# Optimization experiments

Hardware: AMD Instinct MI355X
Metric: run time of the kernel (lower is better)

The kernel has to match this reference:

```python
import jax, jax.numpy as jnp
import numpy as np

F_DIM, P_DIM, H_DIM, N_EXP = 768, 512, 1024, 4
B, T = 8192, 8192


def _gelu(x):
    return jax.nn.gelu(x, approximate=False)


def _normalize(x, eps=1e-12):
    n = jnp.linalg.norm(x, axis=-1, keepdims=True)
    return x / jnp.maximum(n, eps)


def setup_inputs() -> dict:
    key = jax.random.key(0)
    ks = jax.random.split(key, 24)
    s = 0.02
    inp = {
        'image_features': jax.random.normal(ks[0], (B, F_DIM), jnp.float32),
        'text_features': jax.random.normal(ks[1], (B, F_DIM), jnp.float32),
        'target_features': jax.random.normal(ks[2], (T, F_DIM), jnp.float32),
        # projection layers (torch Linear convention: W [out,in])
        'Wt': jax.random.normal(ks[3], (P_DIM, F_DIM), jnp.float32) * s,
        'bt': jnp.zeros((P_DIM,), jnp.float32),
        'Wi': jax.random.normal(ks[4], (P_DIM, F_DIM), jnp.float32) * s,
        'bi': jnp.zeros((P_DIM,), jnp.float32),
        # dynamic scalar MLP: (2P -> H -> 1)
        'ds_W1': jax.random.normal(ks[5], (H_DIM, 2 * P_DIM), jnp.float32) * s,
        'ds_b1': jnp.zeros((H_DIM,), jnp.float32),
        'ds_W2': jax.random.normal(ks[6], (1, H_DIM), jnp.float32) * s,
        'ds_b2': jnp.zeros((1,), jnp.float32),
        # experts stacked: [E, H, 2P]
        'exp_W': jax.random.normal(ks[7], (N_EXP, H_DIM, 2 * P_DIM), jnp.float32) * s,
        'exp_b': jnp.zeros((N_EXP, H_DIM), jnp.float32),
        # router: (2P -> H/4 -> E)
        'rt_W1': jax.random.normal(ks[8], (H_DIM // 4, 2 * P_DIM), jnp.float32) * s,
        'rt_b1': jnp.zeros((H_DIM // 4,), jnp.float32),
        'rt_W2': jax.random.normal(ks[9], (N_EXP, H_DIM // 4), jnp.float32) * s,
        'rt_b2': jnp.zeros((N_EXP,), jnp.float32),
        # output layer: (H -> F)
        'out_W': jax.random.normal(ks[10], (F_DIM, H_DIM), jnp.float32) * s,
        'out_b': jnp.zeros((F_DIM,), jnp.float32),
        'logit_scale': jnp.asarray(np.log(50.0), jnp.float32),
    }
    return inp


def reference(image_features, text_features, target_features, Wt, bt, Wi, bi,
              ds_W1, ds_b1, ds_W2, ds_b2, exp_W, exp_b,
              rt_W1, rt_b1, rt_W2, rt_b2, out_W, out_b, logit_scale):
    # eval mode: all dropouts are identity, no modality drop
    tp = _gelu(text_features @ Wt.T + bt)            # [B,P]
    ip = _gelu(image_features @ Wi.T + bi)           # [B,P]
    comb = jnp.concatenate([tp, ip], axis=-1)        # [B,2P]

    router_logits = _gelu(comb @ rt_W1.T + rt_b1) @ rt_W2.T + rt_b2  # [B,E]
    router_probs = jax.nn.softmax(router_logits, axis=-1)

    expert_out = _gelu(jnp.einsum('bd,ehd->beh', comb, exp_W) + exp_b)  # [B,E,H]
    fused_hidden = jnp.einsum('be,beh->bh', router_probs, expert_out)   # [B,H]
    residual = fused_hidden @ out_W.T + out_b                            # [B,F]

    ds = jax.nn.sigmoid(_gelu(comb @ ds_W1.T + ds_b1) @ ds_W2.T + ds_b2)  # [B,1]
    output = ds * text_features + (1.0 - ds) * image_features + residual
    pred = _normalize(output)
    tgt = _normalize(target_features)
    logits = jnp.exp(logit_scale) * (pred @ tgt.T)   # [B,T]
    return (logits, ds, router_probs)
```

## Files before the change

### kernel.cpp

```cpp
#include <hip/hip_runtime.h>
#include <stdint.h>
#include <math.h>

#define BDIM 8192
#define TDIM 8192
#define FDIM 768
#define PDIM 512
#define HDIM 1024
#define NEXP 4
#define NCAT 5376

using short4v = __attribute__((ext_vector_type(4))) short;
using short8 = __attribute__((ext_vector_type(8))) short;
using f32x4  = __attribute__((ext_vector_type(4))) float;

__device__ __forceinline__ short f2bf(float f) {
  uint32_t u = __builtin_bit_cast(uint32_t, f);
  u += 0x7fffu + ((u >> 16) & 1u);
  return (short)(u >> 16);
}
__device__ __forceinline__ float bf2f(short s) {
  uint32_t u = ((uint32_t)(uint16_t)s) << 16;
  return __builtin_bit_cast(float, u);
}
__device__ __forceinline__ float gelu_exact(float x) {
  return 0.5f * x * (1.0f + erff(x * 0.70710678118654752f));
}

#define GLDS(gp, lp) __builtin_amdgcn_global_load_lds( \
    (const __attribute__((address_space(1))) void*)(gp), \
    (__attribute__((address_space(3))) void*)(lp), 16, 0, 0)

template <int MODE>
__device__ __forceinline__ void gemm_body(
    const short* __restrict__ A, int lda,
    const short* __restrict__ B, int ldb,
    void* __restrict__ C, int ldc, int K,
    const float* __restrict__ bias, float scale,
    int m0, int n0)
{
  __shared__ short sA[4096];
  __shared__ short sB[4096];
  const int t    = threadIdx.x;
  const int lane = t & 63;
  const int wave = t >> 6;
  const int wm = (wave >> 1) * 64;
  const int wn = (wave & 1) * 64;
  const int l15  = lane & 15;
  const int quad = lane >> 4;

  f32x4 acc[4][4];
#pragma unroll
  for (int i = 0; i < 4; ++i)
#pragma unroll
    for (int j = 0; j < 4; ++j)
      acc[i][j] = (f32x4){0.f, 0.f, 0.f, 0.f};

  const int rr = t >> 2;
  const int cc = (t & 3) * 8;
  const short* gA0 = A + (size_t)(m0 + rr) * lda + cc;
  const short* gA1 = A + (size_t)(m0 + 64 + rr) * lda + cc;
  const short* gB0 = B + (size_t)(n0 + rr) * ldb + cc;
  const short* gB1 = B + (size_t)(n0 + 64 + rr) * ldb + cc;
  short* lA0 = sA + t * 8;
  short* lA1 = sA + 2048 + t * 8;
  short* lB0 = sB + t * 8;
  short* lB1 = sB + 2048 + t * 8;

  for (int k0 = 0; k0 < K; k0 += 32) {
    GLDS(gA0 + k0, lA0);
    GLDS(gA1 + k0, lA1);
    GLDS(gB0 + k0, lB0);
    GLDS(gB1 + k0, lB1);
    __syncthreads();
    short8 af[4], bfr[4];
#pragma unroll
    for (int i = 0; i < 4; ++i)
      af[i] = *(const short8*)(sA + (wm + i * 16 + l15) * 32 + quad * 8);
#pragma unroll
    for (int j = 0; j < 4; ++j)
      bfr[j] = *(const short8*)(sB + (wn + j * 16 + l15) * 32 + quad * 8);
#pragma unroll
    for (int i = 0; i < 4; ++i)
#pragma unroll
      for (int j = 0; j < 4; ++j)
        acc[i][j] = __builtin_amdgcn_mfma_f32_16x16x32_bf16(af[i], bfr[j], acc[i][j], 0, 0, 0);
    __syncthreads();
  }

#pragma unroll
  for (int i = 0; i < 4; ++i) {
#pragma unroll
    for (int j = 0; j < 4; ++j) {
      const int col = n0 + wn + j * 16 + l15;
      float bv = (MODE == 2) ? 0.f : bias[col];
#pragma unroll
      for (int r = 0; r < 4; ++r) {
        const int row = m0 + wm + i * 16 + quad * 4 + r;
        float v = acc[i][j][r];
        if (MODE == 0) {
          v = gelu_exact(v + bv);
          ((short*)C)[(size_t)row * ldc + col] = f2bf(v);
        } else if (MODE == 1) {
          ((float*)C)[(size_t)row * ldc + col] = v + bv;
        } else {
          ((float*)C)[(size_t)row * ldc + col] = v * scale;
        }
      }
    }
  }
}

template <int MODE>
__global__ __launch_bounds__(256, 2)
void gemm_bt(const short* __restrict__ A, int lda,
             const short* __restrict__ B, int ldb,
             void* __restrict__ C, int ldc, int K,
             const float* __restrict__ bias,
             const float* __restrict__ scale_ptr)
{
  float scale = 1.f;
  if (MODE == 2) scale = expf(scale_ptr[0]);
  gemm_body<MODE>(A, lda, B, ldb, C, ldc, K, bias, scale,
                  blockIdx.y * 128, blockIdx.x * 128);
}

__global__ __launch_bounds__(256, 2)
void gemm_proj(const short* __restrict__ textb, const short* __restrict__ imgb,
               const short* __restrict__ Wtb, const short* __restrict__ Wib,
               const float* __restrict__ bt, const float* __restrict__ bi,
               short* __restrict__ comb)
{
  const int z = blockIdx.z;
  const short* A = z ? imgb : textb;
  const short* B = z ? Wib : Wtb;
  const float* bias = z ? bi : bt;
  short* C = comb + (z ? 512 : 0);
  gemm_body<0>(A, FDIM, B, FDIM, C, 1024, FDIM, bias, 1.f,
               blockIdx.y * 128, blockIdx.x * 128);
}

#define SEG0 1572864u
#define SEG1 3145728u
#define SEG2 3244032u
#define SEG3 3342336u
#define SEG4 4390912u
#define SEG5 4653056u
#define SEG6 4718592u
#define SEG7 4915200u
#define SEG8 4916544u

__global__ __launch_bounds__(256)
void prep_all(const float* __restrict__ text, const float* __restrict__ image,
              const float* __restrict__ Wt, const float* __restrict__ Wi,
              const float* __restrict__ exp_W, const float* __restrict__ ds_W1,
              const float* __restrict__ rt_W1, const float* __restrict__ out_W,
              const float* __restrict__ exp_b, const float* __restrict__ ds_b1,
              const float* __restrict__ rt_b1,
              short* __restrict__ textb, short* __restrict__ imgb,
              short* __restrict__ Wtb, short* __restrict__ Wib,
              short* __restrict__ Bcat, short* __restrict__ outWb,
              float* __restrict__ biascat)
{
  const uint32_t i = blockIdx.x * 256 + threadIdx.x;
  if (i >= SEG8) return;
  if (i >= SEG7) {
    const uint32_t j = (i - SEG7) * 4;
#pragma unroll
    for (int k = 0; k < 4; ++k) {
      uint32_t idx = j + k;
      float v;
      if (idx < 4096)      v = exp_b[idx];
      else if (idx < 5120) v = ds_b1[idx - 4096];
      else                 v = rt_b1[idx - 5120];
      biascat[idx] = v;
    }
    return;
  }
  const float* s;
  short* d;
  uint32_t j;
  if (i < SEG1) {
    if (i < SEG0) { j = i;        s = text;  d = textb; }
    else          { j = i - SEG0; s = image; d = imgb;  }
  } else if (i < SEG3) {
    if (i < SEG2) { j = i - SEG1; s = Wt; d = Wtb; }
    else          { j = i - SEG2; s = Wi; d = Wib; }
  } else if (i < SEG5) {
    if (i < SEG4) { j = i - SEG3; s = exp_W; d = Bcat; }
    else          { j = i - SEG4; s = ds_W1; d = Bcat + (size_t)4096 * 1024; }
  } else {
    if (i < SEG6) { j = i - SEG5; s = rt_W1; d = Bcat + (size_t)5120 * 1024; }
    else          { j = i - SEG6; s = out_W; d = outWb; }
  }
  float4 v = ((const float4*)s)[j];
  short4v o = { f2bf(v.x), f2bf(v.y), f2bf(v.z), f2bf(v.w) };
  ((short4v*)d)[j] = o;
}

__global__ __launch_bounds__(256)
void moe_mix(const short* __restrict__ Hall,
             const float* __restrict__ rt_W2, const float* __restrict__ rt_b2,
             const float* __restrict__ ds_W2, const float* __restrict__ ds_b2,
             float* __restrict__ out_probs, float* __restrict__ out_ds,
             short* __restrict__ fused)
{
  const int b = blockIdx.x;
  const int t = threadIdx.x;
  const int lane = t & 63;
  const int wave = t >> 6;
  const short* h = Hall + (size_t)b * NCAT;

  float rv = bf2f(h[5120 + t]);
  float p0 = rv * rt_W2[t];
  float p1 = rv * rt_W2[256 + t];
  float p2 = rv * rt_W2[512 + t];
  float p3 = rv * rt_W2[768 + t];
  float dd = 0.f;
#pragma unroll
  for (int k = 0; k < 4; ++k)
    dd += bf2f(h[4096 + k * 256 + t]) * ds_W2[k * 256 + t];

#pragma unroll
  for (int off = 32; off; off >>= 1) {
    p0 += __shfl_xor(p0, off);
    p1 += __shfl_xor(p1, off);
    p2 += __shfl_xor(p2, off);
    p3 += __shfl_xor(p3, off);
    dd += __shfl_xor(dd, off);
  }
  __shared__ float red[5][4];
  __shared__ float bc[5];
  if (lane == 0) {
    red[0][wave] = p0; red[1][wave] = p1; red[2][wave] = p2;
    red[3][wave] = p3; red[4][wave] = dd;
  }
  __syncthreads();
  if (t == 0) {
    float l0 = red[0][0] + red[0][1] + red[0][2] + red[0][3] + rt_b2[0];
    float l1 = red[1][0] + red[1][1] + red[1][2] + red[1][3] + rt_b2[1];
    float l2 = red[2][0] + red[2][1] + red[2][2] + red[2][3] + rt_b2[2];
    float l3 = red[3][0] + red[3][1] + red[3][2] + red[3][3] + rt_b2[3];
    float d  = red[4][0] + red[4][1] + red[4][2] + red[4][3] + ds_b2[0];
    float mx = fmaxf(fmaxf(l0, l1), fmaxf(l2, l3));
    float e0 = expf(l0 - mx), e1 = expf(l1 - mx);
    float e2 = expf(l2 - mx), e3 = expf(l3 - mx);
    float inv = 1.f / (e0 + e1 + e2 + e3);
    bc[0] = e0 * inv; bc[1] = e1 * inv; bc[2] = e2 * inv; bc[3] = e3 * inv;
    bc[4] = 1.f / (1.f + expf(-d));
    out_probs[b * 4 + 0] = bc[0];
    out_probs[b * 4 + 1] = bc[1];
    out_probs[b * 4 + 2] = bc[2];
    out_probs[b * 4 + 3] = bc[3];
    out_ds[b] = bc[4];
  }
  __syncthreads();
  const float q0 = bc[0], q1 = bc[1], q2 = bc[2], q3 = bc[3];
  short* fr = fused + (size_t)b * 1024;
#pragma unroll
  for (int c = t; c < 1024; c += 256) {
    float v = q0 * bf2f(h[c])        + q1 * bf2f(h[1024 + c])
            + q2 * bf2f(h[2048 + c]) + q3 * bf2f(h[3072 + c]);
    fr[c] = f2bf(v);
  }
}

__global__ __launch_bounds__(256)
void normalize_both(const float* __restrict__ text, const float* __restrict__ image,
                    const float* __restrict__ ds, const float* __restrict__ resid,
                    const float* __restrict__ target,
                    short* __restrict__ pred, short* __restrict__ tgtb)
{
  const int bb = blockIdx.x;
  const int t = threadIdx.x;
  float o0, o1, o2;
  short* d;
  if (bb < BDIM) {
    const float dv = ds[bb];
    const float* tx = text + (size_t)bb * FDIM;
    const float* im = image + (size_t)bb * FDIM;
    const float* s  = resid + (size_t)bb * FDIM;
    o0 = dv * tx[t]       + (1.f - dv) * im[t]       + s[t];
    o1 = dv * tx[t + 256] + (1.f - dv) * im[t + 256] + s[t + 256];
    o2 = dv * tx[t + 512] + (1.f - dv) * im[t + 512] + s[t + 512];
    d = pred + (size_t)bb * FDIM;
  } else {
    const int b = bb - BDIM;
    const float* s = target + (size_t)b * FDIM;
    o0 = s[t]; o1 = s[t + 256]; o2 = s[t + 512];
    d = tgtb + (size_t)b * FDIM;
  }
  float ss = o0 * o0 + o1 * o1 + o2 * o2;
  __shared__ float red[4];
#pragma unroll
  for (int off = 32; off; off >>= 1) ss += __shfl_xor(ss, off);
  if ((t & 63) == 0) red[t >> 6] = ss;
  __syncthreads();
  const float tot = red[0] + red[1] + red[2] + red[3];
  const float rn = 1.f / fmaxf(sqrtf(tot), 1e-12f);
  d[t]       = f2bf(o0 * rn);
  d[t + 256] = f2bf(o1 * rn);
  d[t + 512] = f2bf(o2 * rn);
}

extern "C" void kernel_launch(void* const* d_in, const int* in_sizes, int n_in,
                              void* d_out, int out_size, void* d_ws, size_t ws_size,
                              hipStream_t stream) {
  const float* image  = (const float*)d_in[0];
  const float* text   = (const float*)d_in[1];
  const float* target = (const float*)d_in[2];
  const float* Wt     = (const float*)d_in[3];
  const float* bt     = (const float*)d_in[4];
  const float* Wi     = (const float*)d_in[5];
  const float* bi     = (const float*)d_in[6];
  const float* ds_W1  = (const float*)d_in[7];
  const float* ds_b1  = (const float*)d_in[8];
  const float* ds_W2  = (const float*)d_in[9];
  const float* ds_b2  = (const float*)d_in[10];
  const float* exp_W  = (const float*)d_in[11];
  const float* exp_b  = (const float*)d_in[12];
  const float* rt_W1  = (const float*)d_in[13];
  const float* rt_b1  = (const float*)d_in[14];
  const float* rt_W2  = (const float*)d_in[15];
  const float* rt_b2  = (const float*)d_in[16];
  const float* out_W  = (const float*)d_in[17];
  const float* out_b  = (const float*)d_in[18];
  const float* logit_scale = (const float*)d_in[19];

  char* ws = (char*)d_ws;
  short* comb  = (short*)ws;  ws += (size_t)BDIM * 1024 * 2;
  short* Hall  = (short*)ws;  ws += (size_t)BDIM * NCAT * 2;
  short* fused = (short*)ws;  ws += (size_t)BDIM * 1024 * 2;
  float* resid = (float*)ws;  ws += (size_t)BDIM * FDIM * 4;
  short* pred  = (short*)ws;  ws += (size_t)BDIM * FDIM * 2;
  short* tgtb  = (short*)ws;  ws += (size_t)TDIM * FDIM * 2;
  short* textb = (short*)ws;  ws += (size_t)BDIM * FDIM * 2;
  short* imgb  = (short*)ws;  ws += (size_t)BDIM * FDIM * 2;
  short* Wtb   = (short*)ws;  ws += (size_t)PDIM * FDIM * 2;
  short* Wib   = (short*)ws;  ws += (size_t)PDIM * FDIM * 2;
  short* outWb = (short*)ws;  ws += (size_t)FDIM * HDIM * 2;
  short* Bcat  = (short*)ws;  ws += (size_t)NCAT * HDIM * 2;
  float* biascat = (float*)ws; ws += (size_t)NCAT * 4;

  float* out_logits = (float*)d_out;
  float* out_ds     = out_logits + (size_t)BDIM * TDIM;
  float* out_probs  = out_ds + BDIM;

  prep_all<<<(SEG8 + 255) / 256, 256, 0, stream>>>(
      text, image, Wt, Wi, exp_W, ds_W1, rt_W1, out_W,
      exp_b, ds_b1, rt_b1,
      textb, imgb, Wtb, Wib, Bcat, outWb, biascat);

  dim3 blk(256);
  gemm_proj<<<dim3(PDIM / 128, BDIM / 128, 2), blk, 0, stream>>>(
      textb, imgb, Wtb, Wib, bt, bi, comb);
  gemm_bt<0><<<dim3(NCAT / 128, BDIM / 128), blk, 0, stream>>>(
      comb, 1024, Bcat, 1024, Hall, NCAT, 1024, biascat, nullptr);
  moe_mix<<<BDIM, 256, 0, stream>>>(Hall, rt_W2, rt_b2, ds_W2, ds_b2,
                                    out_probs, out_ds, fused);
  gemm_bt<1><<<dim3(FDIM / 128, BDIM / 128), blk, 0, stream>>>(
      fused, 1024, outWb, 1024, resid, FDIM, 1024, out_b, nullptr);
  normalize_both<<<BDIM + TDIM, 256, 0, stream>>>(
      text, image, out_ds, resid, target, pred, tgtb);
  gemm_bt<2><<<dim3(TDIM / 128, BDIM / 128), blk, 0, stream>>>(
      pred, FDIM, tgtb, FDIM, out_logits, TDIM, FDIM, nullptr, logit_scale);
}
```

Baseline: 667.7 us.

## Remap GEMM tiles across XCDs and vectorize moe_mix and normalize loads

Adds an XCD-aware block remap to all GEMM launches so that consecutive output tiles land on the same XCD and can share its L2. It also vectorizes the moe_mix and normalize_both kernels to use 4-wide loads and stores, and shrinks normalize blocks to 192 threads. The goal is better L2 locality in the large GEMMs and fewer memory instructions in the elementwise kernels. The remap assumes the grid's tile count divides evenly by 8, which holds for every grid used here.

```diff
diff --git a/kernel.cpp b/kernel.cpp
--- a/kernel.cpp
+++ b/kernel.cpp
@@ -30,6 +30,14 @@
 #define GLDS(gp, lp) __builtin_amdgcn_global_load_lds( \
     (const __attribute__((address_space(1))) void*)(gp), \
     (__attribute__((address_space(3))) void*)(lp), 16, 0, 0)
+
+__device__ __forceinline__ void xcd_remap(int gx, int gy, int& bx, int& by) {
+  const int lin = blockIdx.y * gx + blockIdx.x;
+  const int cpx = (gx * gy) >> 3;
+  const int tl  = (lin & 7) * cpx + (lin >> 3);
+  bx = tl % gx;
+  by = tl / gx;
+}
 
 template <int MODE>
 __device__ __forceinline__ void gemm_body(
@@ -121,8 +129,9 @@
 {
   float scale = 1.f;
   if (MODE == 2) scale = expf(scale_ptr[0]);
-  gemm_body<MODE>(A, lda, B, ldb, C, ldc, K, bias, scale,
-                  blockIdx.y * 128, blockIdx.x * 128);
+  int bx, by;
+  xcd_remap(gridDim.x, gridDim.y, bx, by);
+  gemm_body<MODE>(A, lda, B, ldb, C, ldc, K, bias, scale, by * 128, bx * 128);
 }
 
 __global__ __launch_bounds__(256, 2)
@@ -136,8 +145,9 @@
   const short* B = z ? Wib : Wtb;
   const float* bias = z ? bi : bt;
   short* C = comb + (z ? 512 : 0);
-  gemm_body<0>(A, FDIM, B, FDIM, C, 1024, FDIM, bias, 1.f,
-               blockIdx.y * 128, blockIdx.x * 128);
+  int bx, by;
+  xcd_remap(gridDim.x, gridDim.y, bx, by);
+  gemm_body<0>(A, FDIM, B, FDIM, C, 1024, FDIM, bias, 1.f, by * 128, bx * 128);
 }
 
 #define SEG0 1572864u
@@ -210,16 +220,17 @@
   const int lane = t & 63;
   const int wave = t >> 6;
   const short* h = Hall + (size_t)b * NCAT;
+  const int t4 = t * 4;
 
   float rv = bf2f(h[5120 + t]);
   float p0 = rv * rt_W2[t];
   float p1 = rv * rt_W2[256 + t];
   float p2 = rv * rt_W2[512 + t];
   float p3 = rv * rt_W2[768 + t];
-  float dd = 0.f;
-#pragma unroll
-  for (int k = 0; k < 4; ++k)
-    dd += bf2f(h[4096 + k * 256 + t]) * ds_W2[k * 256 + t];
+  short4v hd = *(const short4v*)(h + 4096 + t4);
+  float4 wd = *(const float4*)(ds_W2 + t4);
+  float dd = bf2f(hd[0]) * wd.x + bf2f(hd[1]) * wd.y
+           + bf2f(hd[2]) * wd.z + bf2f(hd[3]) * wd.w;
 
 #pragma unroll
   for (int off = 32; off; off >>= 1) {
@@ -256,16 +267,21 @@
   }
   __syncthreads();
   const float q0 = bc[0], q1 = bc[1], q2 = bc[2], q3 = bc[3];
-  short* fr = fused + (size_t)b * 1024;
-#pragma unroll
-  for (int c = t; c < 1024; c += 256) {
-    float v = q0 * bf2f(h[c])        + q1 * bf2f(h[1024 + c])
-            + q2 * bf2f(h[2048 + c]) + q3 * bf2f(h[3072 + c]);
-    fr[c] = f2bf(v);
-  }
-}
-
-__global__ __launch_bounds__(256)
+  short4v a0 = *(const short4v*)(h + t4);
+  short4v a1 = *(const short4v*)(h + 1024 + t4);
+  short4v a2 = *(const short4v*)(h + 2048 + t4);
+  short4v a3 = *(const short4v*)(h + 3072 + t4);
+  short4v o;
+#pragma unroll
+  for (int k = 0; k < 4; ++k) {
+    float v = q0 * bf2f(a0[k]) + q1 * bf2f(a1[k])
+            + q2 * bf2f(a2[k]) + q3 * bf2f(a3[k]);
+    o[k] = f2bf(v);
+  }
+  *(short4v*)(fused + (size_t)b * 1024 + t4) = o;
+}
+
+__global__ __launch_bounds__(192)
 void normalize_both(const float* __restrict__ text, const float* __restrict__ image,
                     const float* __restrict__ ds, const float* __restrict__ resid,
                     const float* __restrict__ target,
@@ -273,34 +289,33 @@
 {
   const int bb = blockIdx.x;
   const int t = threadIdx.x;
-  float o0, o1, o2;
+  float4 o;
   short* d;
   if (bb < BDIM) {
     const float dv = ds[bb];
-    const float* tx = text + (size_t)bb * FDIM;
-    const float* im = image + (size_t)bb * FDIM;
-    const float* s  = resid + (size_t)bb * FDIM;
-    o0 = dv * tx[t]       + (1.f - dv) * im[t]       + s[t];
-    o1 = dv * tx[t + 256] + (1.f - dv) * im[t + 256] + s[t + 256];
-    o2 = dv * tx[t + 512] + (1.f - dv) * im[t + 512] + s[t + 512];
+    const float4 a = ((const float4*)(text  + (size_t)bb * FDIM))[t];
+    const float4 m = ((const float4*)(image + (size_t)bb * FDIM))[t];
+    const float4 s = ((const float4*)(resid + (size_t)bb * FDIM))[t];
+    o.x = dv * a.x + (1.f - dv) * m.x + s.x;
+    o.y = dv * a.y + (1.f - dv) * m.y + s.y;
+    o.z = dv * a.z + (1.f - dv) * m.z + s.z;
+    o.w = dv * a.w + (1.f - dv) * m.w + s.w;
     d = pred + (size_t)bb * FDIM;
   } else {
     const int b = bb - BDIM;
-    const float* s = target + (size_t)b * FDIM;
-    o0 = s[t]; o1 = s[t + 256]; o2 = s[t + 512];
+    o = ((const float4*)(target + (size_t)b * FDIM))[t];
     d = tgtb + (size_t)b * FDIM;
   }
-  float ss = o0 * o0 + o1 * o1 + o2 * o2;
-  __shared__ float red[4];
+  float ss = o.x * o.x + o.y * o.y + o.z * o.z + o.w * o.w;
+  __shared__ float red[3];
 #pragma unroll
   for (int off = 32; off; off >>= 1) ss += __shfl_xor(ss, off);
   if ((t & 63) == 0) red[t >> 6] = ss;
   __syncthreads();
-  const float tot = red[0] + red[1] + red[2] + red[3];
+  const float tot = red[0] + red[1] + red[2];
   const float rn = 1.f / fmaxf(sqrtf(tot), 1e-12f);
-  d[t]       = f2bf(o0 * rn);
-  d[t + 256] = f2bf(o1 * rn);
-  d[t + 512] = f2bf(o2 * rn);
+  short4v r = { f2bf(o.x * rn), f2bf(o.y * rn), f2bf(o.z * rn), f2bf(o.w * rn) };
+  ((short4v*)d)[t] = r;
 }
 
 extern "C" void kernel_launch(void* const* d_in, const int* in_sizes, int n_in,
@@ -360,7 +375,7 @@
                                     out_probs, out_ds, fused);
   gemm_bt<1><<<dim3(FDIM / 128, BDIM / 128), blk, 0, stream>>>(
       fused, 1024, outWb, 1024, resid, FDIM, 1024, out_b, nullptr);
-  normalize_both<<<BDIM + TDIM, 256, 0, stream>>>(
+  normalize_both<<<BDIM + TDIM, 192, 0, stream>>>(
       text, image, out_ds, resid, target, pred, tgtb);
   gemm_bt<2><<<dim3(TDIM / 128, BDIM / 128), blk, 0, stream>>>(
       pred, FDIM, tgtb, FDIM, out_logits, TDIM, FDIM, nullptr, logit_scale);
```

Result: slower. 700.9 us (+5.0%).
